# Optimization experiments

Measured on AMD Instinct MI355X. Metric: run time of the kernel, lower is better.

Reference implementation:

```python
import jax, jax.numpy as jnp
import numpy as np

L, D, HID, QH, KVH, V, B, S, R = 2, 1024, 4096, 16, 4, 32000, 2, 2048, 20
HEAD, G = D // QH, QH // KVH
ALPHA, THETA = 32.0, 50000.0


def setup_inputs() -> dict:
    key = jax.random.key(0)
    ks = iter(jax.random.split(key, 40))
    def w(shape, s=0.02):
        return jax.random.normal(next(ks), shape, jnp.float32) * s
    KD = KVH * HEAD
    return {
        'xs': jax.random.randint(next(ks), (B, S), 0, V, dtype=jnp.int32),
        'emb': w((V, D)),
        'Wq': w((L, D, D)), 'bq': w((L, D)),
        'Wk': w((L, D, KD)), 'bk': w((L, KD)),
        'Wv': w((L, D, KD)), 'bv': w((L, KD)),
        'Wo': w((L, D, D)), 'bo': w((L, D)),
        'att_scale': 1.0 + w((L, D)),
        'mlp_scale': 1.0 + w((L, D)),
        'final_scale': 1.0 + w((D,)),
        'W1': w((L, D, HID)), 'A1': w((L, D, R)), 'a1b': w((L, R)), 'B1': w((L, R, HID)), 'b1b': w((L, HID)),
        'W2': w((L, D, HID)), 'A2': w((L, D, R)), 'a2b': w((L, R)), 'B2': w((L, R, HID)), 'b2b': w((L, HID)),
        'W3': w((L, HID, D)), 'A3': w((L, HID, R)), 'a3b': w((L, R)), 'B3': w((L, R, D)), 'b3b': w((L, D)),
        'startpos': 0,
    }


def _rms(x, scale):
    return scale * x * jax.lax.rsqrt(jnp.mean(x * x, axis=-1, keepdims=True) + 1e-5)


def _lora(x, Wl, Aw, ab, Bw, bb):
    # base linear output is detached in the original (no grad through it)
    return jax.lax.stop_gradient(x @ Wl) + ((x @ Aw + ab) @ Bw + bb) / ALPHA


def _forward(xs, startpos, emb, Wq, bq, Wk, bk, Wv, bv, Wo, bo,
             att_scale, mlp_scale, final_scale,
             W1, A1, a1b, B1, b1b, W2, A2, a2b, B2, b2b, W3, A3, a3b, B3, b3b):
    x = emb[xs]  # (B,S,D)
    # RoPE tables (head dim = D//QH, pairs rotated as complex numbers)
    freqs = 1.0 / THETA ** (jnp.arange(0, HEAD, 2, dtype=jnp.float32) / HEAD)  # (HEAD//2,)
    pos = jnp.arange(startpos, startpos + S, dtype=jnp.float32)
    ang = pos[:, None] * freqs[None, :]  # (S, HEAD//2)
    cos, sin = jnp.cos(ang), jnp.sin(ang)

    def rope(t):  # t: (B,S,H,HEAD)
        tr = t.reshape(t.shape[:-1] + (HEAD // 2, 2))
        t0, t1 = tr[..., 0], tr[..., 1]
        c, s = cos[None, :, None, :], sin[None, :, None, :]
        return jnp.stack((t0 * c - t1 * s, t0 * s + t1 * c), axis=-1).reshape(t.shape)

    causal = jnp.arange(S)[None, :] <= jnp.arange(S)[:, None]  # (Sq, Skv)
    inv_sqrt_d = np.float32(1.0 / np.sqrt(HEAD))
    for l in range(L):
        h = _rms(x, att_scale[l])
        q = rope((h @ Wq[l] + bq[l]).reshape(B, S, QH, HEAD))
        k = rope((h @ Wk[l] + bk[l]).reshape(B, S, KVH, HEAD))
        v = (h @ Wv[l] + bv[l]).reshape(B, S, KVH, HEAD)
        # GQA: q heads grouped per kv head (q head i uses kv head i//G); no explicit KV repeat
        qg = q.reshape(B, S, KVH, G, HEAD)
        scores = jnp.einsum('bskgd,btkd->bkgst', qg, k) * inv_sqrt_d
        if startpos == 0:
            scores = jnp.where(causal[None, None, None], scores, -jnp.inf)
        attn = jax.nn.softmax(scores, axis=-1)
        o = jnp.einsum('bkgst,btkd->bskgd', attn, v).reshape(B, S, D)
        x = x + (o @ Wo[l] + bo[l])
        h2 = _rms(x, mlp_scale[l])
        m = _lora(h2, W1[l], A1[l], a1b[l], B1[l], b1b[l]) * jax.nn.silu(
            _lora(h2, W2[l], A2[l], a2b[l], B2[l], b2b[l]))
        x = x + _lora(m, W3[l], A3[l], a3b[l], B3[l], b3b[l])
    f = _rms(x, final_scale)
    return f @ emb.T  # tied logits (B,S,V)


def reference(xs, emb, Wq, bq, Wk, bk, Wv, bv, Wo, bo, att_scale, mlp_scale, final_scale,
              W1, A1, a1b, B1, b1b, W2, A2, a2b, B2, b2b, W3, A3, a3b, B3, b3b, startpos):
    return _forward(xs, startpos, emb, Wq, bq, Wk, bk, Wv, bv, Wo, bo,
                    att_scale, mlp_scale, final_scale,
                    W1, A1, a1b, B1, b1b, W2, A2, a2b, B2, b2b, W3, A3, a3b, B3, b3b)
```

## Files before the change

kernel.cpp:

```cpp
#include <hip/hip_runtime.h>
#include <hip/hip_bf16.h>
#include <math.h>

constexpr int L_   = 2;
constexpr int D_   = 1024;
constexpr int HID_ = 4096;
constexpr int QH_  = 16;
constexpr int KVH_ = 4;
constexpr int V_   = 32000;
constexpr int B_   = 2;
constexpr int S_   = 2048;
constexpr int R_   = 20;
constexpr int HEAD_ = D_ / QH_;
constexpr int KD_   = KVH_ * HEAD_;
constexpr int QKV_  = D_ + 2 * KD_;
constexpr int M_    = B_ * S_;
constexpr float INV_ALPHA_ = 1.0f / 32.0f;
constexpr float LOG_STEP_ = 0.3381180865f;

typedef unsigned short ushort_t;
typedef __attribute__((ext_vector_type(8))) short bf16x8;
typedef __attribute__((ext_vector_type(4))) float f32x4;
typedef __attribute__((address_space(1))) const unsigned int gas_u32;
typedef __attribute__((address_space(3))) unsigned int las_u32;

__device__ __forceinline__ void gload16(const void* g, void* l) {
  __builtin_amdgcn_global_load_lds((gas_u32*)g, (las_u32*)l, 16, 0, 0);
}

__device__ __forceinline__ ushort_t f2bf(float f) {
  union { float f; unsigned int u; } c; c.f = f;
  unsigned int u = c.u + 0x7FFFu + ((c.u >> 16) & 1u);
  return (ushort_t)(u >> 16);
}
__device__ __forceinline__ float bflo(unsigned int w) {
  union { unsigned int u; float f; } c; c.u = w << 16; return c.f;
}
__device__ __forceinline__ float bfhi(unsigned int w) {
  union { unsigned int u; float f; } c; c.u = w & 0xFFFF0000u; return c.f;
}

__global__ __launch_bounds__(256) void k_embed(const int* __restrict__ xs,
                                               const float* __restrict__ emb,
                                               float* __restrict__ x) {
  int i = blockIdx.x * blockDim.x + threadIdx.x;
  int total4 = M_ * D_ / 4;
  if (i >= total4) return;
  int row = i >> 8;
  int c4  = i & 255;
  const float4* src = reinterpret_cast<const float4*>(emb + (size_t)xs[row] * D_) + c4;
  reinterpret_cast<float4*>(x)[i] = *src;
}

__global__ __launch_bounds__(256) void k_rms(const float* __restrict__ x,
                                             const float* __restrict__ scale,
                                             ushort_t* __restrict__ out) {
  int row = blockIdx.x;
  const float* xr = x + (size_t)row * D_;
  float ss = 0.f;
  for (int i = threadIdx.x; i < D_; i += 256) { float v = xr[i]; ss += v * v; }
  for (int off = 32; off > 0; off >>= 1) ss += __shfl_down(ss, off);
  __shared__ float red[5];
  if ((threadIdx.x & 63) == 0) red[threadIdx.x >> 6] = ss;
  __syncthreads();
  if (threadIdx.x == 0)
    red[4] = rsqrtf((red[0] + red[1] + red[2] + red[3]) * (1.0f / D_) + 1e-5f);
  __syncthreads();
  float inv = red[4];
  ushort_t* orow = out + (size_t)row * D_;
  for (int i = threadIdx.x; i < D_; i += 256) orow[i] = f2bf(scale[i] * xr[i] * inv);
}

__global__ __launch_bounds__(256) void k_cast(const float* __restrict__ in,
                                              ushort_t* __restrict__ out, int n8) {
  int i = blockIdx.x * blockDim.x + threadIdx.x;
  if (i >= n8) return;
  const float4* p = reinterpret_cast<const float4*>(in) + i * 2;
  float4 a = p[0], b = p[1];
  ushort_t r[8] = { f2bf(a.x), f2bf(a.y), f2bf(a.z), f2bf(a.w),
                    f2bf(b.x), f2bf(b.y), f2bf(b.z), f2bf(b.w) };
  reinterpret_cast<uint4*>(out)[i] = *reinterpret_cast<uint4*>(r);
}

__global__ __launch_bounds__(256) void k_tcast(const float* __restrict__ in,
                                               ushort_t* __restrict__ out,
                                               int K, int N) {
  __shared__ float t[32][33];
  int n0 = blockIdx.x * 32, k0 = blockIdx.y * 32;
  int c = threadIdx.x & 31, r0 = threadIdx.x >> 5;
#pragma unroll
  for (int rr = 0; rr < 4; ++rr) {
    int r = r0 + rr * 8;
    t[r][c] = in[(size_t)(k0 + r) * N + n0 + c];
  }
  __syncthreads();
#pragma unroll
  for (int rr = 0; rr < 4; ++rr) {
    int r = r0 + rr * 8;
    out[(size_t)(n0 + r) * K + k0 + c] = f2bf(t[c][r]);
  }
}

__global__ __launch_bounds__(256) void k_qkvbias(const float* __restrict__ bq,
                                                 const float* __restrict__ bk,
                                                 const float* __restrict__ bv,
                                                 float* __restrict__ b) {
  int i = blockIdx.x * 256 + threadIdx.x;
  if (i >= QKV_) return;
  b[i] = i < D_ ? bq[i] : (i < D_ + KD_ ? bk[i - D_] : bv[i - D_ - KD_]);
}

__global__ __launch_bounds__(256) void k_ropeprep_k(const float* __restrict__ qkv,
                                                    ushort_t* __restrict__ Kb) {
  int i = blockIdx.x * 256 + threadIdx.x;
  int pi = i & 31;
  int kh = (i >> 5) & 3;
  int s  = (i >> 7) & (S_ - 1);
  int b  = i >> 18;
  float freq = expf(-LOG_STEP_ * (float)pi);
  float ang = (float)s * freq;
  float sn, cs;
  sincosf(ang, &sn, &cs);
  const float* p = qkv + (size_t)(b * S_ + s) * QKV_ + D_ + kh * 64 + 2 * pi;
  float t0 = p[0], t1 = p[1];
  ushort_t* q = Kb + (size_t)((b * KVH_ + kh) * S_ + s) * 64 + 2 * pi;
  q[0] = f2bf(t0 * cs - t1 * sn);
  q[1] = f2bf(t0 * sn + t1 * cs);
}

__global__ __launch_bounds__(256) void k_prep_v(const float* __restrict__ qkv,
                                                ushort_t* __restrict__ Vt) {
  __shared__ float t[32][33];
  int s0 = blockIdx.x * 32, d0 = blockIdx.y * 32, bkh = blockIdx.z;
  int c = threadIdx.x & 31, r0 = threadIdx.x >> 5;
#pragma unroll
  for (int rr = 0; rr < 4; ++rr) {
    int r = r0 + rr * 8;
    t[r][c] = qkv[(size_t)((bkh >> 2) * S_ + s0 + r) * QKV_ + D_ + KD_ + (bkh & 3) * 64 + d0 + c];
  }
  __syncthreads();
#pragma unroll
  for (int rr = 0; rr < 4; ++rr) {
    int r = r0 + rr * 8;
    Vt[(size_t)(bkh * 64 + d0 + r) * S_ + s0 + c] = f2bf(t[c][r]);
  }
}

__global__ __launch_bounds__(256) void k_attn3(const float* __restrict__ qkv,
                                               const ushort_t* __restrict__ Kb,
                                               const ushort_t* __restrict__ Vt,
                                               ushort_t* __restrict__ obf) {
  __shared__ ushort_t Ks[128 * 64];
  __shared__ ushort_t Vs[64 * 128];
  __shared__ ushort_t Ps[4][16 * 128];

  int bid = blockIdx.x;
  int qt = 31 - (bid & 31);
  int qh = (bid >> 5) & 15;
  int b  = bid >> 9;
  int kh = qh >> 2;
  int tid = threadIdx.x;
  int w = tid >> 6, lane = tid & 63;
  int q0 = qt * 64;

  const ushort_t* Kbh = Kb + (size_t)(b * KVH_ + kh) * S_ * 64;
  const ushort_t* Vth = Vt + (size_t)(b * KVH_ + kh) * 64 * S_;

  const int rsel = lane & 15;
  const int g4 = lane >> 4;

  bf16x8 qa[2];
  {
    int pos = q0 + w * 16 + rsel;
    const float* qp = qkv + (size_t)(b * S_ + pos) * QKV_ + qh * 64 + g4 * 8;
#pragma unroll
    for (int kk = 0; kk < 2; ++kk) {
      float4 f0 = *reinterpret_cast<const float4*>(qp + kk * 32);
      float4 f1 = *reinterpret_cast<const float4*>(qp + kk * 32 + 4);
      float f[8] = {f0.x, f0.y, f0.z, f0.w, f1.x, f1.y, f1.z, f1.w};
      int dbase = g4 * 8 + kk * 32;
      ushort_t tq[8];
#pragma unroll
      for (int p = 0; p < 4; ++p) {
        int pi = (dbase >> 1) + p;
        float freq = expf(-LOG_STEP_ * (float)pi);
        float ang = (float)pos * freq;
        float sn, cs;
        sincosf(ang, &sn, &cs);
        float t0 = f[2 * p], t1 = f[2 * p + 1];
        tq[2 * p]     = f2bf((t0 * cs - t1 * sn) * 0.125f);
        tq[2 * p + 1] = f2bf((t0 * sn + t1 * cs) * 0.125f);
      }
      qa[kk] = *reinterpret_cast<const bf16x8*>(tq);
    }
  }

  f32x4 oacc[4];
#pragma unroll
  for (int j = 0; j < 4; ++j) oacc[j] = {0.f, 0.f, 0.f, 0.f};
  float m[4] = {-1e30f, -1e30f, -1e30f, -1e30f};
  float l[4] = {0.f, 0.f, 0.f, 0.f};

  for (int t0 = 0; t0 < q0 + 64; t0 += 128) {
#pragma unroll
    for (int q = 0; q < 4; ++q) {
      int item = q * 64 + lane;
      int row = w * 32 + (item >> 3);
      int slot = item & 7;
      const char* gk = (const char*)Kbh + (size_t)(t0 + row) * 128 + ((slot ^ (row & 7)) << 4);
      gload16(gk, (char*)Ks + (size_t)w * 4096 + q * 1024);
    }
#pragma unroll
    for (int q = 0; q < 4; ++q) {
      int item = q * 64 + lane;
      int row = w * 16 + (item >> 4);
      int slot = item & 15;
      const char* gv = (const char*)Vth + (size_t)row * (S_ * 2) + (size_t)t0 * 2 + ((slot ^ (row & 7)) << 4);
      gload16(gv, (char*)Vs + (size_t)w * 4096 + q * 1024);
    }
    __syncthreads();

    f32x4 sacc[8];
#pragma unroll
    for (int j = 0; j < 8; ++j) sacc[j] = {0.f, 0.f, 0.f, 0.f};
#pragma unroll
    for (int kk = 0; kk < 2; ++kk) {
#pragma unroll
      for (int j = 0; j < 8; ++j) {
        int krow = j * 16 + rsel;
        int chunk = kk * 4 + g4;
        bf16x8 kf = *reinterpret_cast<const bf16x8*>(
            &Ks[krow * 64 + ((chunk ^ (krow & 7)) << 3)]);
        sacc[j] = __builtin_amdgcn_mfma_f32_16x16x32_bf16(qa[kk], kf, sacc[j], 0, 0, 0);
      }
    }
    if (t0 + 127 > q0) {
#pragma unroll
      for (int j = 0; j < 8; ++j)
#pragma unroll
        for (int e = 0; e < 4; ++e) {
          int keyg = t0 + j * 16 + rsel;
          int qg = q0 + w * 16 + g4 * 4 + e;
          if (keyg > qg) sacc[j][e] = -1e30f;
        }
    }

    float corr[4];
#pragma unroll
    for (int e = 0; e < 4; ++e) {
      float mt = sacc[0][e];
#pragma unroll
      for (int j = 1; j < 8; ++j) mt = fmaxf(mt, sacc[j][e]);
#pragma unroll
      for (int off = 1; off < 16; off <<= 1) mt = fmaxf(mt, __shfl_xor(mt, off));
      float mn = fmaxf(m[e], mt);
      corr[e] = __expf(m[e] - mn);
      m[e] = mn;
    }
    float rs[4] = {0.f, 0.f, 0.f, 0.f};
#pragma unroll
    for (int j = 0; j < 8; ++j)
#pragma unroll
      for (int e = 0; e < 4; ++e) {
        float p = __expf(sacc[j][e] - m[e]);
        sacc[j][e] = p;
        rs[e] += p;
      }
#pragma unroll
    for (int e = 0; e < 4; ++e) {
#pragma unroll
      for (int off = 1; off < 16; off <<= 1) rs[e] += __shfl_xor(rs[e], off);
      l[e] = l[e] * corr[e] + rs[e];
    }
#pragma unroll
    for (int j = 0; j < 4; ++j)
#pragma unroll
      for (int e = 0; e < 4; ++e) oacc[j][e] *= corr[e];

#pragma unroll
    for (int j = 0; j < 8; ++j)
#pragma unroll
      for (int e = 0; e < 4; ++e) {
        int prow = g4 * 4 + e;
        int pcol = j * 16 + rsel;
        Ps[w][prow * 128 + (((pcol >> 3) ^ (prow & 7)) << 3) + (pcol & 7)] = f2bf(sacc[j][e]);
      }

    bf16x8 pa[4];
#pragma unroll
    for (int kk = 0; kk < 4; ++kk) {
      int chunk = kk * 4 + g4;
      pa[kk] = *reinterpret_cast<const bf16x8*>(
          &Ps[w][rsel * 128 + ((chunk ^ (rsel & 7)) << 3)]);
    }
#pragma unroll
    for (int kk = 0; kk < 4; ++kk) {
#pragma unroll
      for (int jd = 0; jd < 4; ++jd) {
        int vrow = jd * 16 + rsel;
        int chunk = kk * 4 + g4;
        bf16x8 vf = *reinterpret_cast<const bf16x8*>(
            &Vs[vrow * 128 + ((chunk ^ (vrow & 7)) << 3)]);
        oacc[jd] = __builtin_amdgcn_mfma_f32_16x16x32_bf16(pa[kk], vf, oacc[jd], 0, 0, 0);
      }
    }
    __syncthreads();
  }

#pragma unroll
  for (int e = 0; e < 4; ++e) {
    int tok = b * S_ + q0 + w * 16 + g4 * 4 + e;
    float inv = 1.f / l[e];
#pragma unroll
    for (int jd = 0; jd < 4; ++jd) {
      int col = qh * 64 + jd * 16 + rsel;
      obf[(size_t)tok * D_ + col] = f2bf(oacc[jd][e] * inv);
    }
  }
}

__global__ __launch_bounds__(256) void k_silumul(const ushort_t* __restrict__ g1,
                                                 const ushort_t* __restrict__ g2,
                                                 ushort_t* __restrict__ out) {
  int i = blockIdx.x * 256 + threadIdx.x;
  uint4 a4 = reinterpret_cast<const uint4*>(g1)[i];
  uint4 b4 = reinterpret_cast<const uint4*>(g2)[i];
  unsigned au[4] = {a4.x, a4.y, a4.z, a4.w};
  unsigned bu[4] = {b4.x, b4.y, b4.z, b4.w};
  ushort_t r[8];
#pragma unroll
  for (int q = 0; q < 4; ++q) {
    float a0 = bflo(au[q]), a1 = bfhi(au[q]);
    float b0 = bflo(bu[q]), b1 = bfhi(bu[q]);
    r[2 * q]     = f2bf(a0 * b0 / (1.f + __expf(-b0)));
    r[2 * q + 1] = f2bf(a1 * b1 / (1.f + __expf(-b1)));
  }
  reinterpret_cast<uint4*>(out)[i] = *reinterpret_cast<uint4*>(r);
}

__global__ __launch_bounds__(256) void k_trA(const float* __restrict__ A,
                                             ushort_t* __restrict__ At, int K) {
  int idx = blockIdx.x * 256 + threadIdx.x;
  if (idx >= K * R_) return;
  int k = idx / R_, r = idx - k * R_;
  At[(size_t)r * K + k] = f2bf(A[idx]);
}

template <int K>
__global__ __launch_bounds__(256) void k_loraA(const ushort_t* __restrict__ hbm,
                                               const ushort_t* __restrict__ At,
                                               const float* __restrict__ ab,
                                               float* __restrict__ u) {
  constexpr int E = K / 64;
  int row = blockIdx.x * 4 + (threadIdx.x >> 6);
  int lane = threadIdx.x & 63;
  float hf[E];
  {
    const uint4* hp = reinterpret_cast<const uint4*>(hbm + (size_t)row * K + lane * E);
#pragma unroll
    for (int i = 0; i < E / 8; ++i) {
      uint4 vv = hp[i];
      unsigned int wsv[4] = {vv.x, vv.y, vv.z, vv.w};
#pragma unroll
      for (int q = 0; q < 4; ++q) {
        hf[i * 8 + q * 2]     = bflo(wsv[q]);
        hf[i * 8 + q * 2 + 1] = bfhi(wsv[q]);
      }
    }
  }
  for (int r = 0; r < R_; ++r) {
    const uint4* ap = reinterpret_cast<const uint4*>(At + (size_t)r * K + lane * E);
    float acc = 0.f;
#pragma unroll
    for (int i = 0; i < E / 8; ++i) {
      uint4 av = ap[i];
      unsigned int wsv[4] = {av.x, av.y, av.z, av.w};
#pragma unroll
      for (int q = 0; q < 4; ++q) {
        acc = fmaf(hf[i * 8 + q * 2], bflo(wsv[q]), acc);
        acc = fmaf(hf[i * 8 + q * 2 + 1], bfhi(wsv[q]), acc);
      }
    }
#pragma unroll
    for (int off = 1; off < 64; off <<= 1) acc += __shfl_xor(acc, off);
    if (lane == 0) u[(size_t)row * R_ + r] = acc + ab[r];
  }
}

template <bool LORA, bool OBF>
__global__ __launch_bounds__(256) void k_bgemm(const ushort_t* __restrict__ A,
                                               const ushort_t* __restrict__ Bt,
                                               const float* __restrict__ bias,
                                               const float* __restrict__ u,
                                               const float* __restrict__ Bl,
                                               const float* __restrict__ lb,
                                               const float* __restrict__ Cin,
                                               void* __restrict__ Cout,
                                               int M, int N, int K) {
  __shared__ ushort_t lds[3][2][128 * 32];
  const int tid = threadIdx.x;
  const int lane = tid & 63;
  const int w = tid >> 6;
  const int wr = w >> 1, wc = w & 1;

  unsigned nwg = gridDim.x * gridDim.y;
  unsigned orig = blockIdx.y * gridDim.x + blockIdx.x;
  unsigned qq = nwg >> 3, r8 = nwg & 7;
  unsigned xcd = orig & 7, loc = orig >> 3;
  unsigned swz = (xcd < r8 ? xcd * (qq + 1) : r8 * (qq + 1) + (xcd - r8) * qq) + loc;
  const int bm = (int)(swz / gridDim.x) * 128;
  const int bn = (int)(swz % gridDim.x) * 128;

  f32x4 acc[4][4];
#pragma unroll
  for (int i = 0; i < 4; ++i)
#pragma unroll
    for (int j = 0; j < 4; ++j) acc[i][j] = {0.f, 0.f, 0.f, 0.f};

  const int srow = (lane >> 2);
  const int skcol = (lane & 3) * 8;
  const int nt = K >> 5;

#define STAGE_TILE(kt)                                                          \
  {                                                                             \
    int k0_ = (kt) * 32;                                                        \
    int sl_ = (kt) % 3;                                                         \
    _Pragma("unroll")                                                           \
    for (int q_ = 0; q_ < 2; ++q_) {                                            \
      int c_ = w * 2 + q_;                                                      \
      gload16(A + (size_t)(bm + c_ * 16 + srow) * K + k0_ + skcol,              \
              (char*)&lds[sl_][0][0] + c_ * 1024);                              \
      gload16(Bt + (size_t)(bn + c_ * 16 + srow) * K + k0_ + skcol,             \
              (char*)&lds[sl_][1][0] + c_ * 1024);                              \
    }                                                                           \
  }

  STAGE_TILE(0)
  STAGE_TILE(1)
  asm volatile("s_waitcnt vmcnt(4)\n\ts_barrier" ::: "memory");

  const int koff = (lane >> 4) * 8;
  const int rsel = lane & 15;

  for (int t = 0; t < nt; ++t) {
    if (t + 2 < nt) STAGE_TILE(t + 2)
    const ushort_t* As = &lds[t % 3][0][0];
    const ushort_t* Bs = &lds[t % 3][1][0];
    bf16x8 af[4], bfr[4];
#pragma unroll
    for (int i = 0; i < 4; ++i)
      af[i] = *reinterpret_cast<const bf16x8*>(&As[(wr * 64 + i * 16 + rsel) * 32 + koff]);
#pragma unroll
    for (int j = 0; j < 4; ++j)
      bfr[j] = *reinterpret_cast<const bf16x8*>(&Bs[(wc * 64 + j * 16 + rsel) * 32 + koff]);
    __builtin_amdgcn_s_setprio(1);
#pragma unroll
    for (int i = 0; i < 4; ++i)
#pragma unroll
      for (int j = 0; j < 4; ++j)
        acc[i][j] = __builtin_amdgcn_mfma_f32_16x16x32_bf16(af[i], bfr[j], acc[i][j], 0, 0, 0);
    __builtin_amdgcn_s_setprio(0);
    if (t + 2 < nt) {
      asm volatile("s_waitcnt vmcnt(4)\n\ts_barrier" ::: "memory");
    } else if (t + 1 < nt) {
      asm volatile("s_waitcnt vmcnt(0)\n\ts_barrier" ::: "memory");
    }
  }
#undef STAGE_TILE

  float* Cf = (float*)Cout;
  ushort_t* Cb = (ushort_t*)Cout;

  if constexpr (LORA) {
    asm volatile("s_barrier" ::: "memory");
    float* Us  = (float*)&lds[0][0][0];
    float* Bls = (float*)&lds[1][0][0];
    for (int t = tid; t < 128 * R_; t += 256) {
      Us[t] = u[(size_t)bm * R_ + t];
      int rr = t >> 7, nn = t & 127;
      Bls[t] = Bl[(size_t)rr * N + bn + nn];
    }
    __syncthreads();
#pragma unroll
    for (int i = 0; i < 4; ++i) {
      int rl0 = wr * 64 + i * 16 + (lane >> 4) * 4;
#pragma unroll
      for (int e = 0; e < 4; ++e) {
        int rl = rl0 + e;
        float u20[R_];
#pragma unroll
        for (int r = 0; r < R_; ++r) u20[r] = Us[rl * R_ + r];
#pragma unroll
        for (int j = 0; j < 4; ++j) {
          int cl = wc * 64 + j * 16 + (lane & 15);
          float ud = lb[bn + cl];
#pragma unroll
          for (int r = 0; r < R_; ++r) ud = fmaf(u20[r], Bls[r * 128 + cl], ud);
          int row = bm + rl, col = bn + cl;
          float vv = acc[i][j][e] + ud * INV_ALPHA_;
          if constexpr (OBF) {
            Cb[(size_t)row * N + col] = f2bf(vv);
          } else {
            if (Cin) vv += Cin[(size_t)row * N + col];
            Cf[(size_t)row * N + col] = vv;
          }
        }
      }
    }
  } else {
#pragma unroll
    for (int i = 0; i < 4; ++i) {
      int row0 = bm + wr * 64 + i * 16 + (lane >> 4) * 4;
#pragma unroll
      for (int j = 0; j < 4; ++j) {
        int col = bn + wc * 64 + j * 16 + (lane & 15);
        float bv = bias ? bias[col] : 0.f;
#pragma unroll
        for (int e = 0; e < 4; ++e) {
          int row = row0 + e;
          float vv = acc[i][j][e] + bv;
          if constexpr (OBF) {
            Cb[(size_t)row * N + col] = f2bf(vv);
          } else {
            if (Cin) vv += Cin[(size_t)row * N + col];
            Cf[(size_t)row * N + col] = vv;
          }
        }
      }
    }
  }
}

template <bool LORA, bool OBF>
__global__ __launch_bounds__(512, 2) void k_bgemm3(const ushort_t* __restrict__ A,
                                                   const ushort_t* __restrict__ Bt,
                                                   const float* __restrict__ bias,
                                                   const float* __restrict__ u,
                                                   const float* __restrict__ Bl,
                                                   const float* __restrict__ lb,
                                                   const float* __restrict__ Cin,
                                                   void* __restrict__ Cout,
                                                   int M, int N, int K) {
  __shared__ ushort_t lds[2][32768];
  const int tid = threadIdx.x;
  const int lane = tid & 63;
  const int w = tid >> 6;
  const int wr = w >> 2;
  const int wc = w & 3;

  unsigned nwg = gridDim.x * gridDim.y;
  unsigned orig = blockIdx.y * gridDim.x + blockIdx.x;
  unsigned qq = nwg >> 3, r8 = nwg & 7;
  unsigned xcd = orig & 7, loc = orig >> 3;
  unsigned swz = (xcd < r8 ? xcd * (qq + 1) : r8 * (qq + 1) + (xcd - r8) * qq) + loc;
  const int bm = (int)(swz / gridDim.x) * 256;
  const int bn = (int)(swz % gridDim.x) * 256;

  f32x4 acc[8][4];
#pragma unroll
  for (int i = 0; i < 8; ++i)
#pragma unroll
    for (int j = 0; j < 4; ++j) acc[i][j] = {0.f, 0.f, 0.f, 0.f};

  const int srow8 = lane >> 3;
  const int scol  = ((lane & 7) ^ srow8) * 8;
  const int nt = K >> 6;

#define STAGE3(kt)                                                              \
  {                                                                             \
    int k0_ = (kt) << 6;                                                        \
    int sl_ = (kt) & 1;                                                         \
    _Pragma("unroll")                                                           \
    for (int c_ = 0; c_ < 4; ++c_) {                                            \
      int ch = w * 4 + c_;                                                      \
      gload16(A + (size_t)(bm + ch * 8 + srow8) * K + k0_ + scol,               \
              (char*)&lds[sl_][0] + ch * 1024);                                 \
    }                                                                           \
    _Pragma("unroll")                                                           \
    for (int c_ = 0; c_ < 4; ++c_) {                                            \
      int ch = w * 4 + c_;                                                      \
      gload16(Bt + (size_t)(bn + ch * 8 + srow8) * K + k0_ + scol,              \
              (char*)&lds[sl_][16384] + ch * 1024);                             \
    }                                                                           \
  }

  STAGE3(0)
  STAGE3(1)
  asm volatile("s_waitcnt vmcnt(8)\n\ts_barrier" ::: "memory");

  const int rsel = lane & 15;
  const int g4 = lane >> 4;

  for (int t = 0; t < nt; ++t) {
    const ushort_t* As = &lds[t & 1][0];
    const ushort_t* Bs = &lds[t & 1][16384];
#pragma unroll
    for (int kk = 0; kk < 2; ++kk) {
      int slotA = kk * 4 + g4;
      bf16x8 af[8], bfr[4];
#pragma unroll
      for (int fm = 0; fm < 8; ++fm) {
        int row = wr * 128 + fm * 16 + rsel;
        af[fm] = *reinterpret_cast<const bf16x8*>(&As[row * 64 + ((slotA ^ (row & 7)) << 3)]);
      }
#pragma unroll
      for (int fn = 0; fn < 4; ++fn) {
        int row = wc * 64 + fn * 16 + rsel;
        bfr[fn] = *reinterpret_cast<const bf16x8*>(&Bs[row * 64 + ((slotA ^ (row & 7)) << 3)]);
      }
      __builtin_amdgcn_s_setprio(1);
#pragma unroll
      for (int fm = 0; fm < 8; ++fm)
#pragma unroll
        for (int fn = 0; fn < 4; ++fn)
          acc[fm][fn] = __builtin_amdgcn_mfma_f32_16x16x32_bf16(af[fm], bfr[fn], acc[fm][fn], 0, 0, 0);
      __builtin_amdgcn_s_setprio(0);
    }
    asm volatile("s_barrier" ::: "memory");
    if (t + 2 < nt) {
      STAGE3(t + 2)
      asm volatile("s_waitcnt vmcnt(8)\n\ts_barrier" ::: "memory");
    } else if (t + 1 < nt) {
      asm volatile("s_waitcnt vmcnt(0)\n\ts_barrier" ::: "memory");
    }
  }
#undef STAGE3

  float* Cf = (float*)Cout;
  ushort_t* Cb = (ushort_t*)Cout;

  if constexpr (LORA) {
    asm volatile("s_barrier" ::: "memory");
    float* Us  = (float*)&lds[0][0];
    float* Bls = (float*)&lds[1][0];
    for (int t2 = tid; t2 < 256 * R_; t2 += 512) Us[t2] = u[(size_t)bm * R_ + t2];
    for (int t2 = tid; t2 < R_ * 256; t2 += 512) {
      int rr = t2 >> 8, nn = t2 & 255;
      Bls[t2] = Bl[(size_t)rr * N + bn + nn];
    }
    __syncthreads();
#pragma unroll
    for (int fm = 0; fm < 8; ++fm) {
      int rl0 = wr * 128 + fm * 16 + g4 * 4;
#pragma unroll
      for (int e = 0; e < 4; ++e) {
        int rl = rl0 + e;
        float u20[R_];
#pragma unroll
        for (int r = 0; r < R_; ++r) u20[r] = Us[rl * R_ + r];
#pragma unroll
        for (int fn = 0; fn < 4; ++fn) {
          int cl = wc * 64 + fn * 16 + rsel;
          float ud = lb[bn + cl];
#pragma unroll
          for (int r = 0; r < R_; ++r) ud = fmaf(u20[r], Bls[r * 256 + cl], ud);
          int row = bm + rl, col = bn + cl;
          float vv = acc[fm][fn][e] + ud * INV_ALPHA_;
          if constexpr (OBF) {
            Cb[(size_t)row * N + col] = f2bf(vv);
          } else {
            if (Cin) vv += Cin[(size_t)row * N + col];
            Cf[(size_t)row * N + col] = vv;
          }
        }
      }
    }
  } else {
#pragma unroll
    for (int fm = 0; fm < 8; ++fm) {
      int row0 = bm + wr * 128 + fm * 16 + g4 * 4;
#pragma unroll
      for (int fn = 0; fn < 4; ++fn) {
        int col = bn + wc * 64 + fn * 16 + rsel;
        float bv = bias ? bias[col] : 0.f;
#pragma unroll
        for (int e = 0; e < 4; ++e) {
          int row = row0 + e;
          float vv = acc[fm][fn][e] + bv;
          if constexpr (OBF) {
            Cb[(size_t)row * N + col] = f2bf(vv);
          } else {
            if (Cin) vv += Cin[(size_t)row * N + col];
            Cf[(size_t)row * N + col] = vv;
          }
        }
      }
    }
  }
}

static inline void bgemm(hipStream_t st, const ushort_t* A, const ushort_t* Bt,
                         const float* bias, const float* Cin, float* C,
                         int M, int N, int K) {
  dim3 g(N / 128, M / 128);
  k_bgemm<false, false><<<g, 256, 0, st>>>(A, Bt, bias, nullptr, nullptr, nullptr, Cin, C, M, N, K);
}
static inline void bgemm_lora_f32(hipStream_t st, const ushort_t* A, const ushort_t* Bt,
                                  const float* u, const float* Bl, const float* lb,
                                  const float* Cin, float* C, int M, int N, int K) {
  dim3 g(N / 128, M / 128);
  k_bgemm<true, false><<<g, 256, 0, st>>>(A, Bt, nullptr, u, Bl, lb, Cin, C, M, N, K);
}
static inline void bgemm3(hipStream_t st, const ushort_t* A, const ushort_t* Bt,
                          const float* bias, const float* Cin, float* C,
                          int M, int N, int K) {
  dim3 g(N / 256, M / 256);
  k_bgemm3<false, false><<<g, 512, 0, st>>>(A, Bt, bias, nullptr, nullptr, nullptr, Cin, C, M, N, K);
}
static inline void bgemm3_lora_bf(hipStream_t st, const ushort_t* A, const ushort_t* Bt,
                                  const float* u, const float* Bl, const float* lb,
                                  ushort_t* C, int M, int N, int K) {
  dim3 g(N / 256, M / 256);
  k_bgemm3<true, true><<<g, 512, 0, st>>>(A, Bt, nullptr, u, Bl, lb, nullptr, C, M, N, K);
}
static inline void tcast(hipStream_t st, const float* in, ushort_t* out, int K, int N) {
  dim3 g(N / 32, K / 32);
  k_tcast<<<g, 256, 0, st>>>(in, out, K, N);
}

extern "C" void kernel_launch(void* const* d_in, const int* in_sizes, int n_in,
                              void* d_out, int out_size, void* d_ws, size_t ws_size,
                              hipStream_t stream) {
  (void)in_sizes; (void)n_in; (void)out_size; (void)ws_size;
  const int*   xs  = (const int*)d_in[0];
  const float* emb = (const float*)d_in[1];
  const float* Wq  = (const float*)d_in[2];
  const float* bq  = (const float*)d_in[3];
  const float* Wk  = (const float*)d_in[4];
  const float* bk  = (const float*)d_in[5];
  const float* Wv  = (const float*)d_in[6];
  const float* bv  = (const float*)d_in[7];
  const float* Wo  = (const float*)d_in[8];
  const float* bo  = (const float*)d_in[9];
  const float* att_scale   = (const float*)d_in[10];
  const float* mlp_scale   = (const float*)d_in[11];
  const float* final_scale = (const float*)d_in[12];
  const float* W1  = (const float*)d_in[13];
  const float* A1  = (const float*)d_in[14];
  const float* a1b = (const float*)d_in[15];
  const float* B1  = (const float*)d_in[16];
  const float* b1b = (const float*)d_in[17];
  const float* W2  = (const float*)d_in[18];
  const float* A2  = (const float*)d_in[19];
  const float* a2b = (const float*)d_in[20];
  const float* B2  = (const float*)d_in[21];
  const float* b2b = (const float*)d_in[22];
  const float* W3  = (const float*)d_in[23];
  const float* A3  = (const float*)d_in[24];
  const float* a3b = (const float*)d_in[25];
  const float* B3  = (const float*)d_in[26];
  const float* b3b = (const float*)d_in[27];
  float* out = (float*)d_out;

  float* ws   = (float*)d_ws;
  float* xbuf = ws;
  float* qkv  = xbuf + (size_t)M_ * D_;
  float* ubuf = qkv + (size_t)M_ * QKV_;
  float* qkvb = ubuf + (size_t)M_ * R_;
  ushort_t* g1b = (ushort_t*)(qkvb + QKV_);
  ushort_t* g2b = g1b + (size_t)M_ * HID_;
  ushort_t* hb  = g2b + (size_t)M_ * HID_;
  ushort_t* wT  = hb + (size_t)M_ * HID_;
  ushort_t* At  = wT + (size_t)HID_ * D_;
  ushort_t* embT = At + (size_t)R_ * HID_;
  ushort_t* Kb = g1b;
  ushort_t* Vt = Kb + (size_t)B_ * KVH_ * S_ * 64;

  k_embed<<<dim3(M_ * D_ / 4 / 256), dim3(256), 0, stream>>>(xs, emb, xbuf);

  for (int l = 0; l < L_; ++l) {
    k_rms<<<dim3(M_), dim3(256), 0, stream>>>(xbuf, att_scale + (size_t)l * D_, hb);
    tcast(stream, Wq + (size_t)l * D_ * D_, wT, D_, D_);
    tcast(stream, Wk + (size_t)l * D_ * KD_, wT + (size_t)D_ * D_, D_, KD_);
    tcast(stream, Wv + (size_t)l * D_ * KD_, wT + (size_t)(D_ + KD_) * D_, D_, KD_);
    k_qkvbias<<<dim3(6), dim3(256), 0, stream>>>(bq + (size_t)l * D_, bk + (size_t)l * KD_,
                                                 bv + (size_t)l * KD_, qkvb);
    bgemm(stream, hb, wT, qkvb, nullptr, qkv, M_, QKV_, D_);
    {
      int npk = M_ * KVH_ * 32;
      k_ropeprep_k<<<dim3(npk / 256), dim3(256), 0, stream>>>(qkv, Kb);
    }
    k_prep_v<<<dim3(S_ / 32, 2, B_ * KVH_), dim3(256), 0, stream>>>(qkv, Vt);
    k_attn3<<<dim3(B_ * QH_ * (S_ / 64)), dim3(256), 0, stream>>>(qkv, Kb, Vt, hb);
    tcast(stream, Wo + (size_t)l * D_ * D_, wT, D_, D_);
    bgemm(stream, hb, wT, bo + (size_t)l * D_, xbuf, xbuf, M_, D_, D_);

    k_rms<<<dim3(M_), dim3(256), 0, stream>>>(xbuf, mlp_scale + (size_t)l * D_, hb);
    k_trA<<<dim3((D_ * R_ + 255) / 256), dim3(256), 0, stream>>>(A1 + (size_t)l * D_ * R_, At, D_);
    k_loraA<D_><<<dim3(M_ / 4), dim3(256), 0, stream>>>(hb, At, a1b + (size_t)l * R_, ubuf);
    tcast(stream, W1 + (size_t)l * D_ * HID_, wT, D_, HID_);
    bgemm3_lora_bf(stream, hb, wT, ubuf, B1 + (size_t)l * R_ * HID_, b1b + (size_t)l * HID_,
                   g1b, M_, HID_, D_);
    k_trA<<<dim3((D_ * R_ + 255) / 256), dim3(256), 0, stream>>>(A2 + (size_t)l * D_ * R_, At, D_);
    k_loraA<D_><<<dim3(M_ / 4), dim3(256), 0, stream>>>(hb, At, a2b + (size_t)l * R_, ubuf);
    tcast(stream, W2 + (size_t)l * D_ * HID_, wT, D_, HID_);
    bgemm3_lora_bf(stream, hb, wT, ubuf, B2 + (size_t)l * R_ * HID_, b2b + (size_t)l * HID_,
                   g2b, M_, HID_, D_);
    k_silumul<<<dim3(M_ * HID_ / 8 / 256), dim3(256), 0, stream>>>(g1b, g2b, hb);
    k_trA<<<dim3((HID_ * R_ + 255) / 256), dim3(256), 0, stream>>>(A3 + (size_t)l * HID_ * R_, At, HID_);
    k_loraA<HID_><<<dim3(M_ / 4), dim3(256), 0, stream>>>(hb, At, a3b + (size_t)l * R_, ubuf);
    tcast(stream, W3 + (size_t)l * HID_ * D_, wT, HID_, D_);
    bgemm_lora_f32(stream, hb, wT, ubuf, B3 + (size_t)l * R_ * D_, b3b + (size_t)l * D_,
                   xbuf, xbuf, M_, D_, HID_);
  }

  k_rms<<<dim3(M_), dim3(256), 0, stream>>>(xbuf, final_scale, hb);
  {
    int n8 = (int)((size_t)V_ * D_ / 8);
    k_cast<<<dim3((n8 + 255) / 256), dim3(256), 0, stream>>>(emb, embT, n8);
  }
  bgemm3(stream, hb, embT, nullptr, nullptr, out, M_, V_, D_);
}
```

Measured before the change: 1.459 ms.

## Merge K/V prep kernels, read LoRA A in fp32 directly, halve bgemm3 K-tile

Merges the RoPE-K and V-transpose prep kernels into one launch that branches on block index. It also drops the k_trA transpose-cast kernel, so k_loraA reads the fp32 A matrix directly with strided scalar loads instead of coalesced bf16 vectors. The bgemm3 kernel moves from a 64-wide to a 32-wide K tile with a new LDS swizzle, halving shared memory so more blocks can be resident, at the cost of twice as many barrier and pipeline iterations. Those strided fp32 loads in k_loraA may be less efficient than the old vector loads.

```diff
diff --git a/kernel.cpp b/kernel.cpp
--- a/kernel.cpp
+++ b/kernel.cpp
@@ -110,39 +110,42 @@
   b[i] = i < D_ ? bq[i] : (i < D_ + KD_ ? bk[i - D_] : bv[i - D_ - KD_]);
 }
 
-__global__ __launch_bounds__(256) void k_ropeprep_k(const float* __restrict__ qkv,
-                                                    ushort_t* __restrict__ Kb) {
-  int i = blockIdx.x * 256 + threadIdx.x;
-  int pi = i & 31;
-  int kh = (i >> 5) & 3;
-  int s  = (i >> 7) & (S_ - 1);
-  int b  = i >> 18;
-  float freq = expf(-LOG_STEP_ * (float)pi);
-  float ang = (float)s * freq;
-  float sn, cs;
-  sincosf(ang, &sn, &cs);
-  const float* p = qkv + (size_t)(b * S_ + s) * QKV_ + D_ + kh * 64 + 2 * pi;
-  float t0 = p[0], t1 = p[1];
-  ushort_t* q = Kb + (size_t)((b * KVH_ + kh) * S_ + s) * 64 + 2 * pi;
-  q[0] = f2bf(t0 * cs - t1 * sn);
-  q[1] = f2bf(t0 * sn + t1 * cs);
-}
-
-__global__ __launch_bounds__(256) void k_prep_v(const float* __restrict__ qkv,
-                                                ushort_t* __restrict__ Vt) {
-  __shared__ float t[32][33];
-  int s0 = blockIdx.x * 32, d0 = blockIdx.y * 32, bkh = blockIdx.z;
-  int c = threadIdx.x & 31, r0 = threadIdx.x >> 5;
-#pragma unroll
-  for (int rr = 0; rr < 4; ++rr) {
-    int r = r0 + rr * 8;
-    t[r][c] = qkv[(size_t)((bkh >> 2) * S_ + s0 + r) * QKV_ + D_ + KD_ + (bkh & 3) * 64 + d0 + c];
-  }
-  __syncthreads();
-#pragma unroll
-  for (int rr = 0; rr < 4; ++rr) {
-    int r = r0 + rr * 8;
-    Vt[(size_t)(bkh * 64 + d0 + r) * S_ + s0 + c] = f2bf(t[c][r]);
+__global__ __launch_bounds__(256) void k_prep(const float* __restrict__ qkv,
+                                              ushort_t* __restrict__ Kb,
+                                              ushort_t* __restrict__ Vt) {
+  if (blockIdx.x < 2048) {
+    int i = blockIdx.x * 256 + threadIdx.x;
+    int pi = i & 31;
+    int kh = (i >> 5) & 3;
+    int s  = (i >> 7) & (S_ - 1);
+    int b  = i >> 18;
+    float freq = expf(-LOG_STEP_ * (float)pi);
+    float ang = (float)s * freq;
+    float sn, cs;
+    sincosf(ang, &sn, &cs);
+    const float* p = qkv + (size_t)(b * S_ + s) * QKV_ + D_ + kh * 64 + 2 * pi;
+    float t0 = p[0], t1 = p[1];
+    ushort_t* q = Kb + (size_t)((b * KVH_ + kh) * S_ + s) * 64 + 2 * pi;
+    q[0] = f2bf(t0 * cs - t1 * sn);
+    q[1] = f2bf(t0 * sn + t1 * cs);
+  } else {
+    __shared__ float t[32][33];
+    int idx = blockIdx.x - 2048;
+    int s0 = (idx & 63) * 32;
+    int d0 = ((idx >> 6) & 1) * 32;
+    int bkh = idx >> 7;
+    int c = threadIdx.x & 31, r0 = threadIdx.x >> 5;
+#pragma unroll
+    for (int rr = 0; rr < 4; ++rr) {
+      int r = r0 + rr * 8;
+      t[r][c] = qkv[(size_t)((bkh >> 2) * S_ + s0 + r) * QKV_ + D_ + KD_ + (bkh & 3) * 64 + d0 + c];
+    }
+    __syncthreads();
+#pragma unroll
+    for (int rr = 0; rr < 4; ++rr) {
+      int r = r0 + rr * 8;
+      Vt[(size_t)(bkh * 64 + d0 + r) * S_ + s0 + c] = f2bf(t[c][r]);
+    }
   }
 }
 
@@ -338,17 +341,9 @@
   reinterpret_cast<uint4*>(out)[i] = *reinterpret_cast<uint4*>(r);
 }
 
-__global__ __launch_bounds__(256) void k_trA(const float* __restrict__ A,
-                                             ushort_t* __restrict__ At, int K) {
-  int idx = blockIdx.x * 256 + threadIdx.x;
-  if (idx >= K * R_) return;
-  int k = idx / R_, r = idx - k * R_;
-  At[(size_t)r * K + k] = f2bf(A[idx]);
-}
-
 template <int K>
 __global__ __launch_bounds__(256) void k_loraA(const ushort_t* __restrict__ hbm,
-                                               const ushort_t* __restrict__ At,
+                                               const float* __restrict__ A,
                                                const float* __restrict__ ab,
                                                float* __restrict__ u) {
   constexpr int E = K / 64;
@@ -368,19 +363,12 @@
       }
     }
   }
+  const float* Ab = A + (size_t)(lane * E) * R_;
   for (int r = 0; r < R_; ++r) {
-    const uint4* ap = reinterpret_cast<const uint4*>(At + (size_t)r * K + lane * E);
     float acc = 0.f;
 #pragma unroll
-    for (int i = 0; i < E / 8; ++i) {
-      uint4 av = ap[i];
-      unsigned int wsv[4] = {av.x, av.y, av.z, av.w};
-#pragma unroll
-      for (int q = 0; q < 4; ++q) {
-        acc = fmaf(hf[i * 8 + q * 2], bflo(wsv[q]), acc);
-        acc = fmaf(hf[i * 8 + q * 2 + 1], bfhi(wsv[q]), acc);
-      }
-    }
+    for (int i = 0; i < E; ++i)
+      acc = fmaf(hf[i], Ab[(size_t)i * R_ + r], acc);
 #pragma unroll
     for (int off = 1; off < 64; off <<= 1) acc += __shfl_xor(acc, off);
     if (lane == 0) u[(size_t)row * R_ + r] = acc + ab[r];
@@ -541,7 +529,7 @@
                                                    const float* __restrict__ Cin,
                                                    void* __restrict__ Cout,
                                                    int M, int N, int K) {
-  __shared__ ushort_t lds[2][32768];
+  __shared__ ushort_t lds[2][16384];
   const int tid = threadIdx.x;
   const int lane = tid & 63;
   const int w = tid >> 6;
@@ -562,64 +550,60 @@
 #pragma unroll
     for (int j = 0; j < 4; ++j) acc[i][j] = {0.f, 0.f, 0.f, 0.f};
 
-  const int srow8 = lane >> 3;
-  const int scol  = ((lane & 7) ^ srow8) * 8;
-  const int nt = K >> 6;
+  const int srow16 = lane >> 2;
+  const int sslot  = lane & 3;
+  const int nt = K >> 5;
 
 #define STAGE3(kt)                                                              \
   {                                                                             \
-    int k0_ = (kt) << 6;                                                        \
+    int k0_ = (kt) << 5;                                                        \
     int sl_ = (kt) & 1;                                                         \
     _Pragma("unroll")                                                           \
-    for (int c_ = 0; c_ < 4; ++c_) {                                            \
-      int ch = w * 4 + c_;                                                      \
-      gload16(A + (size_t)(bm + ch * 8 + srow8) * K + k0_ + scol,               \
+    for (int c_ = 0; c_ < 2; ++c_) {                                            \
+      int ch = w * 2 + c_;                                                      \
+      int row = ch * 16 + srow16;                                               \
+      int koff_ = (sslot ^ ((row ^ (row >> 2)) & 3)) << 3;                      \
+      gload16(A + (size_t)(bm + row) * K + k0_ + koff_,                         \
               (char*)&lds[sl_][0] + ch * 1024);                                 \
-    }                                                                           \
-    _Pragma("unroll")                                                           \
-    for (int c_ = 0; c_ < 4; ++c_) {                                            \
-      int ch = w * 4 + c_;                                                      \
-      gload16(Bt + (size_t)(bn + ch * 8 + srow8) * K + k0_ + scol,              \
-              (char*)&lds[sl_][16384] + ch * 1024);                             \
+      gload16(Bt + (size_t)(bn + row) * K + k0_ + koff_,                        \
+              (char*)&lds[sl_][8192] + ch * 1024);                              \
     }                                                                           \
   }
 
   STAGE3(0)
   STAGE3(1)
-  asm volatile("s_waitcnt vmcnt(8)\n\ts_barrier" ::: "memory");
+  asm volatile("s_waitcnt vmcnt(4)\n\ts_barrier" ::: "memory");
 
   const int rsel = lane & 15;
   const int g4 = lane >> 4;
 
   for (int t = 0; t < nt; ++t) {
     const ushort_t* As = &lds[t & 1][0];
-    const ushort_t* Bs = &lds[t & 1][16384];
-#pragma unroll
-    for (int kk = 0; kk < 2; ++kk) {
-      int slotA = kk * 4 + g4;
-      bf16x8 af[8], bfr[4];
-#pragma unroll
-      for (int fm = 0; fm < 8; ++fm) {
-        int row = wr * 128 + fm * 16 + rsel;
-        af[fm] = *reinterpret_cast<const bf16x8*>(&As[row * 64 + ((slotA ^ (row & 7)) << 3)]);
-      }
-#pragma unroll
-      for (int fn = 0; fn < 4; ++fn) {
-        int row = wc * 64 + fn * 16 + rsel;
-        bfr[fn] = *reinterpret_cast<const bf16x8*>(&Bs[row * 64 + ((slotA ^ (row & 7)) << 3)]);
-      }
-      __builtin_amdgcn_s_setprio(1);
-#pragma unroll
-      for (int fm = 0; fm < 8; ++fm)
-#pragma unroll
-        for (int fn = 0; fn < 4; ++fn)
-          acc[fm][fn] = __builtin_amdgcn_mfma_f32_16x16x32_bf16(af[fm], bfr[fn], acc[fm][fn], 0, 0, 0);
-      __builtin_amdgcn_s_setprio(0);
-    }
+    const ushort_t* Bs = &lds[t & 1][8192];
+    bf16x8 af[8], bfr[4];
+#pragma unroll
+    for (int fm = 0; fm < 8; ++fm) {
+      int row = wr * 128 + fm * 16 + rsel;
+      af[fm] = *reinterpret_cast<const bf16x8*>(
+          &As[row * 32 + ((g4 ^ ((row ^ (row >> 2)) & 3)) << 3)]);
+    }
+#pragma unroll
+    for (int fn = 0; fn < 4; ++fn) {
+      int row = wc * 64 + fn * 16 + rsel;
+      bfr[fn] = *reinterpret_cast<const bf16x8*>(
+          &Bs[row * 32 + ((g4 ^ ((row ^ (row >> 2)) & 3)) << 3)]);
+    }
+    __builtin_amdgcn_s_setprio(1);
+#pragma unroll
+    for (int fm = 0; fm < 8; ++fm)
+#pragma unroll
+      for (int fn = 0; fn < 4; ++fn)
+        acc[fm][fn] = __builtin_amdgcn_mfma_f32_16x16x32_bf16(af[fm], bfr[fn], acc[fm][fn], 0, 0, 0);
+    __builtin_amdgcn_s_setprio(0);
     asm volatile("s_barrier" ::: "memory");
     if (t + 2 < nt) {
       STAGE3(t + 2)
-      asm volatile("s_waitcnt vmcnt(8)\n\ts_barrier" ::: "memory");
+      asm volatile("s_waitcnt vmcnt(4)\n\ts_barrier" ::: "memory");
     } else if (t + 1 < nt) {
       asm volatile("s_waitcnt vmcnt(0)\n\ts_barrier" ::: "memory");
     }
@@ -761,8 +745,7 @@
   ushort_t* g2b = g1b + (size_t)M_ * HID_;
   ushort_t* hb  = g2b + (size_t)M_ * HID_;
   ushort_t* wT  = hb + (size_t)M_ * HID_;
-  ushort_t* At  = wT + (size_t)HID_ * D_;
-  ushort_t* embT = At + (size_t)R_ * HID_;
+  ushort_t* embT = wT + (size_t)HID_ * D_;
   ushort_t* Kb = g1b;
   ushort_t* Vt = Kb + (size_t)B_ * KVH_ * S_ * 64;
 
@@ -776,29 +759,25 @@
     k_qkvbias<<<dim3(6), dim3(256), 0, stream>>>(bq + (size_t)l * D_, bk + (size_t)l * KD_,
                                                  bv + (size_t)l * KD_, qkvb);
     bgemm(stream, hb, wT, qkvb, nullptr, qkv, M_, QKV_, D_);
-    {
-      int npk = M_ * KVH_ * 32;
-      k_ropeprep_k<<<dim3(npk / 256), dim3(256), 0, stream>>>(qkv, Kb);
-    }
-    k_prep_v<<<dim3(S_ / 32, 2, B_ * KVH_), dim3(256), 0, stream>>>(qkv, Vt);
+    k_prep<<<dim3(3072), dim3(256), 0, stream>>>(qkv, Kb, Vt);
     k_attn3<<<dim3(B_ * QH_ * (S_ / 64)), dim3(256), 0, stream>>>(qkv, Kb, Vt, hb);
     tcast(stream, Wo + (size_t)l * D_ * D_, wT, D_, D_);
     bgemm(stream, hb, wT, bo + (size_t)l * D_, xbuf, xbuf, M_, D_, D_);
 
     k_rms<<<dim3(M_), dim3(256), 0, stream>>>(xbuf, mlp_scale + (size_t)l * D_, hb);
-    k_trA<<<dim3((D_ * R_ + 255) / 256), dim3(256), 0, stream>>>(A1 + (size_t)l * D_ * R_, At, D_);
-    k_loraA<D_><<<dim3(M_ / 4), dim3(256), 0, stream>>>(hb, At, a1b + (size_t)l * R_, ubuf);
+    k_loraA<D_><<<dim3(M_ / 4), dim3(256), 0, stream>>>(hb, A1 + (size_t)l * D_ * R_,
+                                                        a1b + (size_t)l * R_, ubuf);
     tcast(stream, W1 + (size_t)l * D_ * HID_, wT, D_, HID_);
     bgemm3_lora_bf(stream, hb, wT, ubuf, B1 + (size_t)l * R_ * HID_, b1b + (size_t)l * HID_,
                    g1b, M_, HID_, D_);
-    k_trA<<<dim3((D_ * R_ + 255) / 256), dim3(256), 0, stream>>>(A2 + (size_t)l * D_ * R_, At, D_);
-    k_loraA<D_><<<dim3(M_ / 4), dim3(256), 0, stream>>>(hb, At, a2b + (size_t)l * R_, ubuf);
+    k_loraA<D_><<<dim3(M_ / 4), dim3(256), 0, stream>>>(hb, A2 + (size_t)l * D_ * R_,
+                                                        a2b + (size_t)l * R_, ubuf);
     tcast(stream, W2 + (size_t)l * D_ * HID_, wT, D_, HID_);
     bgemm3_lora_bf(stream, hb, wT, ubuf, B2 + (size_t)l * R_ * HID_, b2b + (size_t)l * HID_,
                    g2b, M_, HID_, D_);
     k_silumul<<<dim3(M_ * HID_ / 8 / 256), dim3(256), 0, stream>>>(g1b, g2b, hb);
-    k_trA<<<dim3((HID_ * R_ + 255) / 256), dim3(256), 0, stream>>>(A3 + (size_t)l * HID_ * R_, At, HID_);
-    k_loraA<HID_><<<dim3(M_ / 4), dim3(256), 0, stream>>>(hb, At, a3b + (size_t)l * R_, ubuf);
+    k_loraA<HID_><<<dim3(M_ / 4), dim3(256), 0, stream>>>(hb, A3 + (size_t)l * HID_ * R_,
+                                                          a3b + (size_t)l * R_, ubuf);
     tcast(stream, W3 + (size_t)l * HID_ * D_, wT, HID_, D_);
     bgemm_lora_f32(stream, hb, wT, ubuf, B3 + (size_t)l * R_ * D_, b3b + (size_t)l * D_,
                    xbuf, xbuf, M_, D_, HID_);
```

Measured after the change: 3.519 ms. 141% more time.
